# Optimization experiments

Hardware: AMD Instinct MI355X
Metric: run time of the kernel (lower is better)

Reference implementation:

```python
import jax, jax.numpy as jnp
import numpy as np

H, W, C = 768, 768, 64


def _segment_ids(mask):
    """mask: [L] int binary separator mask -> [L] int32 segment ids.
    A new grid segment starts at each rising edge (0 -> 1) of the mask;
    pixel 0 always belongs to segment 0. Equivalent to GridStructureBuilder's
    run-based row/column partition, derived via a single cumsum."""
    m = mask.astype(jnp.int32)
    prev = jnp.concatenate([jnp.zeros((1,), jnp.int32), m[:-1]])
    rising = ((m == 1) & (prev == 0)).at[0].set(False)
    return jnp.cumsum(rising.astype(jnp.int32))


def setup_inputs() -> dict:
    key = jax.random.key(0)
    k1, k2, k3 = jax.random.split(key, 3)
    return {
        "input": jax.random.normal(k1, (1, H, W, C), dtype=jnp.float32),
        "h_mask": jax.random.randint(k2, (1, H), 0, 2, dtype=jnp.int32),
        "v_mask": jax.random.randint(k3, (1, W), 0, 2, dtype=jnp.int32),
    }


def reference(input, h_mask, v_mask):
    x = input[0]                      # [H, W, C]
    h, w, c = x.shape
    row_ids = _segment_ids(h_mask[0])  # [H]
    col_ids = _segment_ids(v_mask[0])  # [W]
    # flat cell id per pixel; w is a static upper bound on the column count
    idx = (row_ids[:, None] * w + col_ids[None, :]).reshape(-1)  # [H*W]
    xf = x.reshape(h * w, c)
    n_seg = h * w                      # static upper bound on cell count
    sums = jax.ops.segment_sum(xf, idx, num_segments=n_seg)           # [n_seg, C]
    counts = jax.ops.segment_sum(jnp.ones((h * w,), x.dtype), idx,
                                 num_segments=n_seg)                  # [n_seg]
    # scatter-add of (1/area)*x == per-cell mean
    means = sums / jnp.maximum(counts, 1.0)[:, None]
    # keep_size=True: gather cell means back to every pixel
    return means[idx].reshape(1, h, w, c)
```

## Files before the change

kernel.cpp:

```cpp
#include <hip/hip_runtime.h>


#define GH 768
#define GW 768
#define MAXSEG 385

enum {
    OFF_ROWSTART = 0,
    OFF_ROWEND   = OFF_ROWSTART + MAXSEG,
    OFF_COLSTART = OFF_ROWEND + MAXSEG,
    OFF_COLEND   = OFF_COLSTART + MAXSEG,
    OFF_NROWS    = OFF_COLEND + MAXSEG,
    OFF_NCOLS    = OFF_NROWS + 1,
    OFF_ROWID    = OFF_NCOLS + 1,
    OFF_COLID    = OFF_ROWID + GH,
    OFF_MEANS    = 4096,
};

__global__ __launch_bounds__(768) void seg_scan(const int* __restrict__ h_mask,
                                                const int* __restrict__ v_mask,
                                                int* __restrict__ ws) {
    __shared__ int s[GH];
    const int i = threadIdx.x;
    const bool is_row = (blockIdx.x == 0);
    const int* m = is_row ? h_mask : v_mask;

    int mi = m[i];
    int rising = 0;
    if (i > 0) rising = (mi == 1 && m[i - 1] == 0) ? 1 : 0;
    s[i] = rising;
    __syncthreads();

    for (int off = 1; off < GH; off <<= 1) {
        int add = (i >= off) ? s[i - off] : 0;
        __syncthreads();
        s[i] += add;
        __syncthreads();
    }

    const int seg  = s[i];
    const int segL = (i == 0)      ? -1 : s[i - 1];
    const int segR = (i == GH - 1) ? -2 : s[i + 1];

    ws[(is_row ? OFF_ROWID : OFF_COLID) + i] = seg;

    int* start = ws + (is_row ? OFF_ROWSTART : OFF_COLSTART);
    int* end   = ws + (is_row ? OFF_ROWEND   : OFF_COLEND);
    if (seg != segL) start[seg] = i;
    if (seg != segR) end[seg]   = i + 1;
    if (i == GH - 1) ws[is_row ? OFF_NROWS : OFF_NCOLS] = seg + 1;
}

__global__ __launch_bounds__(256) void cell_mean(const float4* __restrict__ in,
                                                 float4* __restrict__ dst,
                                                 const int* __restrict__ ws,
                                                 int anchor_mode) {
    const int nrows  = ws[OFF_NROWS];
    const int ncols  = ws[OFF_NCOLS];
    const int ncells = nrows * ncols;

    const int wave   = blockIdx.x * 4 + (threadIdx.x >> 6);
    const int nwaves = gridDim.x * 4;
    const int lane   = threadIdx.x & 63;
    const int pg     = lane >> 4;
    const int cq     = lane & 15;

    for (int cell = wave; cell < ncells; cell += nwaves) {
        const int br = cell / ncols;
        const int bc = cell - br * ncols;
        const int y0 = ws[OFF_ROWSTART + br];
        const int y1 = ws[OFF_ROWEND + br];
        const int x0 = ws[OFF_COLSTART + bc];
        const int x1 = ws[OFF_COLEND + bc];
        const int w   = x1 - x0;
        const int npx = w * (y1 - y0);
        const int q16 = 16 / w;
        const int r16 = 16 - q16 * w;

        int wy[4], wx[4];
        #pragma unroll
        for (int k = 0; k < 4; ++k) {
            int t  = x0 + pg + 4 * k;
            int yy = y0;
            while (t >= x1) { t -= w; ++yy; }
            wx[k] = t; wy[k] = yy;
        }

        float4 a0 = make_float4(0.f, 0.f, 0.f, 0.f);
        float4 a1 = a0, a2 = a0, a3 = a0;

        const int nit = (npx + 15) >> 4;
        for (int it = 0; it < nit; ++it) {
            if (wy[0] < y1) { float4 v = in[(wy[0] * GW + wx[0]) * 16 + cq];
                a0.x += v.x; a0.y += v.y; a0.z += v.z; a0.w += v.w; }
            if (wy[1] < y1) { float4 v = in[(wy[1] * GW + wx[1]) * 16 + cq];
                a1.x += v.x; a1.y += v.y; a1.z += v.z; a1.w += v.w; }
            if (wy[2] < y1) { float4 v = in[(wy[2] * GW + wx[2]) * 16 + cq];
                a2.x += v.x; a2.y += v.y; a2.z += v.z; a2.w += v.w; }
            if (wy[3] < y1) { float4 v = in[(wy[3] * GW + wx[3]) * 16 + cq];
                a3.x += v.x; a3.y += v.y; a3.z += v.z; a3.w += v.w; }
            #pragma unroll
            for (int k = 0; k < 4; ++k) {
                wx[k] += r16; wy[k] += q16;
                if (wx[k] >= x1) { wx[k] -= w; wy[k] += 1; }
            }
        }

        float4 acc;
        acc.x = (a0.x + a1.x) + (a2.x + a3.x);
        acc.y = (a0.y + a1.y) + (a2.y + a3.y);
        acc.z = (a0.z + a1.z) + (a2.z + a3.z);
        acc.w = (a0.w + a1.w) + (a2.w + a3.w);
        #pragma unroll
        for (int msk = 16; msk < 64; msk <<= 1) {
            acc.x += __shfl_xor(acc.x, msk, 64);
            acc.y += __shfl_xor(acc.y, msk, 64);
            acc.z += __shfl_xor(acc.z, msk, 64);
            acc.w += __shfl_xor(acc.w, msk, 64);
        }

        if (lane < 16) {
            const float inv = 1.f / (float)npx;
            float4 mean = make_float4(acc.x * inv, acc.y * inv,
                                      acc.z * inv, acc.w * inv);
            const int oidx = anchor_mode ? (y0 * GW + x0) * 16 + lane
                                         : cell * 16 + lane;
            dst[oidx] = mean;
        }
    }
}

__global__ __launch_bounds__(256) void bcast_ws(float4* __restrict__ out,
                                                const float4* __restrict__ means,
                                                const int* __restrict__ ws) {
    const int ncols = ws[OFF_NCOLS];
    int g = blockIdx.x * 256 + threadIdx.x;
    #pragma unroll 3
    for (int it = 0; it < 18; ++it, g += 2048 * 256) {
        const int p  = g >> 4;
        const int cq = g & 15;
        const int y  = p / GW;
        const int x  = p - y * GW;
        const int rid = ws[OFF_ROWID + y];
        const int cid = ws[OFF_COLID + x];
        out[g] = means[(rid * ncols + cid) * 16 + cq];
    }
}

__global__ __launch_bounds__(256) void bcast_anchor(float4* out,
                                                    const int* __restrict__ ws) {
    int g = blockIdx.x * 256 + threadIdx.x;
    for (int it = 0; it < 18; ++it, g += 2048 * 256) {
        const int p  = g >> 4;
        const int cq = g & 15;
        const int y  = p / GW;
        const int x  = p - y * GW;
        const int rid = ws[OFF_ROWID + y];
        const int cid = ws[OFF_COLID + x];
        const int ya  = ws[OFF_ROWSTART + rid];
        const int xa  = ws[OFF_COLSTART + cid];
        out[g] = out[(ya * GW + xa) * 16 + cq];
    }
}

extern "C" void kernel_launch(void* const* d_in, const int* in_sizes, int n_in,
                              void* d_out, int out_size, void* d_ws, size_t ws_size,
                              hipStream_t stream) {
    const float* in  = (const float*)d_in[0];
    const int* hmask = (const int*)d_in[1];
    const int* vmask = (const int*)d_in[2];
    float* out = (float*)d_out;
    int* ws = (int*)d_ws;

    seg_scan<<<2, GH, 0, stream>>>(hmask, vmask, ws);

    const size_t need = (size_t)OFF_MEANS * 4
                      + (size_t)MAXSEG * MAXSEG * 64 * 4;
    if (ws_size >= need) {
        float4* means = (float4*)(ws + OFF_MEANS);
        cell_mean<<<2048, 256, 0, stream>>>((const float4*)in, means, ws, 0);
        bcast_ws<<<2048, 256, 0, stream>>>((float4*)out, means, ws);
    } else {
        cell_mean<<<2048, 256, 0, stream>>>((const float4*)in, (float4*)out, ws, 1);
        bcast_anchor<<<2048, 256, 0, stream>>>((float4*)out, ws);
    }
}
```

Baseline: 283.8 us.

## Process two cells per wave with prefetched bounds and nontemporal loads

The cell-mean kernel now has each wave handle two cells at once, A and B. Each cell's pixels are split into contiguous chunks across the four lane groups, and the bounds of the next pair are prefetched while the current pair is being summed. Loads are issued unconditionally, with clamped coordinates and predicated accumulation, and use nontemporal hints; the broadcast kernel switches to nontemporal stores with a larger unroll. The goal is more memory-level parallelism and less dependent index arithmetic, at the cost of extra register pressure and wasted loads on small cells.

```diff
diff --git a/kernel.cpp b/kernel.cpp
--- a/kernel.cpp
+++ b/kernel.cpp
@@ -4,6 +4,8 @@
 #define GH 768
 #define GW 768
 #define MAXSEG 385
+
+typedef __attribute__((ext_vector_type(4))) float f32x4;
 
 enum {
     OFF_ROWSTART = 0,
@@ -16,6 +18,7 @@
     OFF_COLID    = OFF_ROWID + GH,
     OFF_MEANS    = 4096,
 };
+#define MEANS_F4 ((size_t)MAXSEG * MAXSEG * 16)
 
 __global__ __launch_bounds__(768) void seg_scan(const int* __restrict__ h_mask,
                                                 const int* __restrict__ v_mask,
@@ -51,10 +54,10 @@
     if (i == GH - 1) ws[is_row ? OFF_NROWS : OFF_NCOLS] = seg + 1;
 }
 
-__global__ __launch_bounds__(256) void cell_mean(const float4* __restrict__ in,
-                                                 float4* __restrict__ dst,
-                                                 const int* __restrict__ ws,
-                                                 int anchor_mode) {
+__global__ __launch_bounds__(256) void cell_mean4(const float4* __restrict__ in,
+                                                  float4* __restrict__ dst,
+                                                  const int* __restrict__ ws,
+                                                  int anchor_mode) {
     const int nrows  = ws[OFF_NROWS];
     const int ncols  = ws[OFF_NCOLS];
     const int ncells = nrows * ncols;
@@ -65,68 +68,136 @@
     const int pg     = lane >> 4;
     const int cq     = lane & 15;
 
-    for (int cell = wave; cell < ncells; cell += nwaves) {
-        const int br = cell / ncols;
-        const int bc = cell - br * ncols;
-        const int y0 = ws[OFF_ROWSTART + br];
-        const int y1 = ws[OFF_ROWEND + br];
-        const int x0 = ws[OFF_COLSTART + bc];
-        const int x1 = ws[OFF_COLEND + bc];
-        const int w   = x1 - x0;
-        const int npx = w * (y1 - y0);
-        const int q16 = 16 / w;
-        const int r16 = 16 - q16 * w;
-
-        int wy[4], wx[4];
+    int cellA = wave;
+    if (cellA >= ncells) return;
+
+    {
+    }
+    int cb0   = (cellA + nwaves < ncells) ? cellA + nwaves : cellA;
+    int brA = cellA / ncols, bcA = cellA - brA * ncols;
+    int brB = cb0   / ncols, bcB = cb0   - brB * ncols;
+    int y0A = ws[OFF_ROWSTART + brA], y1A = ws[OFF_ROWEND + brA];
+    int x0A = ws[OFF_COLSTART + bcA], x1A = ws[OFF_COLEND + bcA];
+    int y0B = ws[OFF_ROWSTART + brB], y1B = ws[OFF_ROWEND + brB];
+    int x0B = ws[OFF_COLSTART + bcB], x1B = ws[OFF_COLEND + bcB];
+
+    while (true) {
+        const bool hasB      = (cellA + nwaves) < ncells;
+        const int  cellB     = hasB ? cellA + nwaves : cellA;
+        const int  nextA     = cellA + 2 * nwaves;
+        const bool have_next = nextA < ncells;
+
+        const int pa  = have_next ? nextA : 0;
+        const int pbn = pa + nwaves;
+        const int pb  = (pbn < ncells) ? pbn : pa;
+        const int nbrA = pa / ncols, nbcA = pa - nbrA * ncols;
+        const int nbrB = pb / ncols, nbcB = pb - nbrB * ncols;
+        const int py0A = ws[OFF_ROWSTART + nbrA], py1A = ws[OFF_ROWEND + nbrA];
+        const int px0A = ws[OFF_COLSTART + nbcA], px1A = ws[OFF_COLEND + nbcA];
+        const int py0B = ws[OFF_ROWSTART + nbrB], py1B = ws[OFF_ROWEND + nbrB];
+        const int px0B = ws[OFF_COLSTART + nbcB], px1B = ws[OFF_COLEND + nbcB];
+
+        const int wA = x1A - x0A, npxA = wA * (y1A - y0A);
+        const int wB = x1B - x0B, npxB = wB * (y1B - y0B);
+        const int qA = (npxA + 3) >> 2, qB = (npxB + 3) >> 2;
+        int lenA = min(pg * qA + qA, npxA) - pg * qA;
+        int lenB = min(pg * qB + qB, npxB) - pg * qB;
+        const int ylimA = y1A - 1, ylimB = y1B - 1;
+
+        const unsigned ubA = (unsigned)(pg * qA);
+        const unsigned uyA = ubA / (unsigned)wA;
+        int yyA = y0A + (int)uyA, xxA = x0A + (int)(ubA - uyA * (unsigned)wA);
+        const unsigned ubB = (unsigned)(pg * qB);
+        const unsigned uyB = ubB / (unsigned)wB;
+        int yyB = y0B + (int)uyB, xxB = x0B + (int)(ubB - uyB * (unsigned)wB);
+
+        float4 accA = make_float4(0.f, 0.f, 0.f, 0.f);
+        float4 accB = make_float4(0.f, 0.f, 0.f, 0.f);
+
+        while (lenA > 0 || lenB > 0) {
+            const int aX0 = xxA;          const int aY0 = min(yyA, ylimA);
+            int aX1 = xxA + 1, aT1 = yyA; if (aX1 >= x1A) { aX1 = x0A; ++aT1; }
+            const int aY1 = min(aT1, ylimA);
+            int aX2 = aX1 + 1, aT2 = aT1; if (aX2 >= x1A) { aX2 = x0A; ++aT2; }
+            const int aY2 = min(aT2, ylimA);
+            int aX3 = aX2 + 1, aT3 = aT2; if (aX3 >= x1A) { aX3 = x0A; ++aT3; }
+            const int aY3 = min(aT3, ylimA);
+            const int bX0 = xxB;          const int bY0 = min(yyB, ylimB);
+            int bX1 = xxB + 1, bT1 = yyB; if (bX1 >= x1B) { bX1 = x0B; ++bT1; }
+            const int bY1 = min(bT1, ylimB);
+            int bX2 = bX1 + 1, bT2 = bT1; if (bX2 >= x1B) { bX2 = x0B; ++bT2; }
+            const int bY2 = min(bT2, ylimB);
+            int bX3 = bX2 + 1, bT3 = bT2; if (bX3 >= x1B) { bX3 = x0B; ++bT3; }
+            const int bY3 = min(bT3, ylimB);
+
+            const f32x4 vA0 = __builtin_nontemporal_load((const f32x4*)&in[(aY0 * GW + aX0) * 16 + cq]);
+            const f32x4 vA1 = __builtin_nontemporal_load((const f32x4*)&in[(aY1 * GW + aX1) * 16 + cq]);
+            const f32x4 vA2 = __builtin_nontemporal_load((const f32x4*)&in[(aY2 * GW + aX2) * 16 + cq]);
+            const f32x4 vA3 = __builtin_nontemporal_load((const f32x4*)&in[(aY3 * GW + aX3) * 16 + cq]);
+            const f32x4 vB0 = __builtin_nontemporal_load((const f32x4*)&in[(bY0 * GW + bX0) * 16 + cq]);
+            const f32x4 vB1 = __builtin_nontemporal_load((const f32x4*)&in[(bY1 * GW + bX1) * 16 + cq]);
+            const f32x4 vB2 = __builtin_nontemporal_load((const f32x4*)&in[(bY2 * GW + bX2) * 16 + cq]);
+            const f32x4 vB3 = __builtin_nontemporal_load((const f32x4*)&in[(bY3 * GW + bX3) * 16 + cq]);
+
+            const bool a0 = (0 < lenA), a1 = (1 < lenA), a2 = (2 < lenA), a3 = (3 < lenA);
+            const bool b0 = (0 < lenB), b1 = (1 < lenB), b2 = (2 < lenB), b3 = (3 < lenB);
+            accA.x += a0 ? vA0.x : 0.f;  accA.y += a0 ? vA0.y : 0.f;
+            accA.z += a0 ? vA0.z : 0.f;  accA.w += a0 ? vA0.w : 0.f;
+            accA.x += a1 ? vA1.x : 0.f;  accA.y += a1 ? vA1.y : 0.f;
+            accA.z += a1 ? vA1.z : 0.f;  accA.w += a1 ? vA1.w : 0.f;
+            accA.x += a2 ? vA2.x : 0.f;  accA.y += a2 ? vA2.y : 0.f;
+            accA.z += a2 ? vA2.z : 0.f;  accA.w += a2 ? vA2.w : 0.f;
+            accA.x += a3 ? vA3.x : 0.f;  accA.y += a3 ? vA3.y : 0.f;
+            accA.z += a3 ? vA3.z : 0.f;  accA.w += a3 ? vA3.w : 0.f;
+            accB.x += b0 ? vB0.x : 0.f;  accB.y += b0 ? vB0.y : 0.f;
+            accB.z += b0 ? vB0.z : 0.f;  accB.w += b0 ? vB0.w : 0.f;
+            accB.x += b1 ? vB1.x : 0.f;  accB.y += b1 ? vB1.y : 0.f;
+            accB.z += b1 ? vB1.z : 0.f;  accB.w += b1 ? vB1.w : 0.f;
+            accB.x += b2 ? vB2.x : 0.f;  accB.y += b2 ? vB2.y : 0.f;
+            accB.z += b2 ? vB2.z : 0.f;  accB.w += b2 ? vB2.w : 0.f;
+            accB.x += b3 ? vB3.x : 0.f;  accB.y += b3 ? vB3.y : 0.f;
+            accB.z += b3 ? vB3.z : 0.f;  accB.w += b3 ? vB3.w : 0.f;
+
+            int aX4 = aX3 + 1, aT4 = aT3; if (aX4 >= x1A) { aX4 = x0A; ++aT4; }
+            xxA = aX4; yyA = aT4;
+            int bX4 = bX3 + 1, bT4 = bT3; if (bX4 >= x1B) { bX4 = x0B; ++bT4; }
+            xxB = bX4; yyB = bT4;
+            lenA -= 4; lenB -= 4;
+        }
+
         #pragma unroll
-        for (int k = 0; k < 4; ++k) {
-            int t  = x0 + pg + 4 * k;
-            int yy = y0;
-            while (t >= x1) { t -= w; ++yy; }
-            wx[k] = t; wy[k] = yy;
+        for (int msk = 16; msk < 64; msk <<= 1) {
+            accA.x += __shfl_xor(accA.x, msk, 64);
+            accA.y += __shfl_xor(accA.y, msk, 64);
+            accA.z += __shfl_xor(accA.z, msk, 64);
+            accA.w += __shfl_xor(accA.w, msk, 64);
+            accB.x += __shfl_xor(accB.x, msk, 64);
+            accB.y += __shfl_xor(accB.y, msk, 64);
+            accB.z += __shfl_xor(accB.z, msk, 64);
+            accB.w += __shfl_xor(accB.w, msk, 64);
         }
 
-        float4 a0 = make_float4(0.f, 0.f, 0.f, 0.f);
-        float4 a1 = a0, a2 = a0, a3 = a0;
-
-        const int nit = (npx + 15) >> 4;
-        for (int it = 0; it < nit; ++it) {
-            if (wy[0] < y1) { float4 v = in[(wy[0] * GW + wx[0]) * 16 + cq];
-                a0.x += v.x; a0.y += v.y; a0.z += v.z; a0.w += v.w; }
-            if (wy[1] < y1) { float4 v = in[(wy[1] * GW + wx[1]) * 16 + cq];
-                a1.x += v.x; a1.y += v.y; a1.z += v.z; a1.w += v.w; }
-            if (wy[2] < y1) { float4 v = in[(wy[2] * GW + wx[2]) * 16 + cq];
-                a2.x += v.x; a2.y += v.y; a2.z += v.z; a2.w += v.w; }
-            if (wy[3] < y1) { float4 v = in[(wy[3] * GW + wx[3]) * 16 + cq];
-                a3.x += v.x; a3.y += v.y; a3.z += v.z; a3.w += v.w; }
-            #pragma unroll
-            for (int k = 0; k < 4; ++k) {
-                wx[k] += r16; wy[k] += q16;
-                if (wx[k] >= x1) { wx[k] -= w; wy[k] += 1; }
+        if (lane < 16) {
+            const float invA = 1.f / (float)npxA;
+            float4 meanA = make_float4(accA.x * invA, accA.y * invA,
+                                       accA.z * invA, accA.w * invA);
+            const int oA = anchor_mode ? (y0A * GW + x0A) * 16 + lane
+                                       : cellA * 16 + lane;
+            dst[oA] = meanA;
+            if (hasB) {
+                const float invB = 1.f / (float)npxB;
+                float4 meanB = make_float4(accB.x * invB, accB.y * invB,
+                                           accB.z * invB, accB.w * invB);
+                const int oB = anchor_mode ? (y0B * GW + x0B) * 16 + lane
+                                           : cellB * 16 + lane;
+                dst[oB] = meanB;
             }
         }
 
-        float4 acc;
-        acc.x = (a0.x + a1.x) + (a2.x + a3.x);
-        acc.y = (a0.y + a1.y) + (a2.y + a3.y);
-        acc.z = (a0.z + a1.z) + (a2.z + a3.z);
-        acc.w = (a0.w + a1.w) + (a2.w + a3.w);
-        #pragma unroll
-        for (int msk = 16; msk < 64; msk <<= 1) {
-            acc.x += __shfl_xor(acc.x, msk, 64);
-            acc.y += __shfl_xor(acc.y, msk, 64);
-            acc.z += __shfl_xor(acc.z, msk, 64);
-            acc.w += __shfl_xor(acc.w, msk, 64);
-        }
-
-        if (lane < 16) {
-            const float inv = 1.f / (float)npx;
-            float4 mean = make_float4(acc.x * inv, acc.y * inv,
-                                      acc.z * inv, acc.w * inv);
-            const int oidx = anchor_mode ? (y0 * GW + x0) * 16 + lane
-                                         : cell * 16 + lane;
-            dst[oidx] = mean;
-        }
+        if (!have_next) break;
+        cellA = nextA;
+        y0A = py0A; y1A = py1A; x0A = px0A; x1A = px1A;
+        y0B = py0B; y1B = py1B; x0B = px0B; x1B = px1B;
     }
 }
 
@@ -135,7 +206,7 @@
                                                 const int* __restrict__ ws) {
     const int ncols = ws[OFF_NCOLS];
     int g = blockIdx.x * 256 + threadIdx.x;
-    #pragma unroll 3
+    #pragma unroll 6
     for (int it = 0; it < 18; ++it, g += 2048 * 256) {
         const int p  = g >> 4;
         const int cq = g & 15;
@@ -143,7 +214,8 @@
         const int x  = p - y * GW;
         const int rid = ws[OFF_ROWID + y];
         const int cid = ws[OFF_COLID + x];
-        out[g] = means[(rid * ncols + cid) * 16 + cq];
+        const float4 v = means[(rid * ncols + cid) * 16 + cq];
+        __builtin_nontemporal_store(*(const f32x4*)&v, (f32x4*)&out[g]);
     }
 }
 
@@ -174,14 +246,13 @@
 
     seg_scan<<<2, GH, 0, stream>>>(hmask, vmask, ws);
 
-    const size_t need = (size_t)OFF_MEANS * 4
-                      + (size_t)MAXSEG * MAXSEG * 64 * 4;
-    if (ws_size >= need) {
+    const size_t need_means = (size_t)OFF_MEANS * 4 + MEANS_F4 * 16;
+    if (ws_size >= need_means) {
         float4* means = (float4*)(ws + OFF_MEANS);
-        cell_mean<<<2048, 256, 0, stream>>>((const float4*)in, means, ws, 0);
+        cell_mean4<<<2048, 256, 0, stream>>>((const float4*)in, means, ws, 0);
         bcast_ws<<<2048, 256, 0, stream>>>((float4*)out, means, ws);
     } else {
-        cell_mean<<<2048, 256, 0, stream>>>((const float4*)in, (float4*)out, ws, 1);
+        cell_mean4<<<2048, 256, 0, stream>>>((const float4*)in, (float4*)out, ws, 1);
         bcast_anchor<<<2048, 256, 0, stream>>>((float4*)out, ws);
     }
 }
```

New measurement: 272.4 us. 4.0% less time.
